# Performance work log

Measured on AMD Instinct MI355X. Metric: run time of the kernel, lower is better.

## Reference

```python
import jax, jax.numpy as jnp
import numpy as np

N_NODES = 50000
N_EDGES = 1600000
IN_FEAT = 48
OUT_FEAT = 48
NUM_RELS = 8


def setup_inputs() -> dict:
    key = jax.random.key(0)
    ks = jax.random.split(key, 9)
    # xavier-ish scale for relu gain
    s1 = float(np.sqrt(2.0) * np.sqrt(6.0 / (IN_FEAT + IN_FEAT)))
    s2 = float(np.sqrt(2.0) * np.sqrt(6.0 / (IN_FEAT + OUT_FEAT)))
    return {
        "inputs": jax.random.normal(ks[0], (N_NODES, IN_FEAT), dtype=jnp.float32),
        "norm": jax.random.uniform(ks[1], (N_EDGES, 1), dtype=jnp.float32),
        "weight1": jax.random.uniform(ks[2], (NUM_RELS, IN_FEAT, IN_FEAT), jnp.float32, -s1, s1),
        "weight2": jax.random.uniform(ks[3], (NUM_RELS, IN_FEAT, OUT_FEAT), jnp.float32, -s2, s2),
        "bias1": jax.random.normal(ks[4], (IN_FEAT,), dtype=jnp.float32) * 0.1,
        "bias2": jax.random.normal(ks[5], (OUT_FEAT,), dtype=jnp.float32) * 0.1,
        "src": jax.random.randint(ks[6], (N_EDGES,), 0, N_NODES, dtype=jnp.int64) if jax.config.jax_enable_x64 else jax.random.randint(ks[6], (N_EDGES,), 0, N_NODES).astype(jnp.int32),
        "dst": jax.random.randint(ks[7], (N_EDGES,), 0, N_NODES).astype(jnp.int32),
        "rel_type": jax.random.randint(ks[8], (N_EDGES,), 0, NUM_RELS).astype(jnp.int32),
    }


def reference(inputs, norm, weight1, weight2, bias1, bias2, src, dst, rel_type):
    # Message depends only on (src node, relation): precompute per (node, rel).
    # Stage 1: h1[n,r,:] = relu(h[n] @ W1[r] + b1)   -> [N, R, in]
    h1 = jax.nn.relu(jnp.einsum('ni,rij->nrj', inputs, weight1) + bias1)
    # Stage 2: h2[n,r,:] = h1[n,r] @ W2[r]           -> [N, R, out]
    h2 = jnp.einsum('nrj,rjo->nro', h1, weight2)
    # Per-edge gather + norm scaling                 -> [E, out]
    msg = h2[src, rel_type] * norm
    # Scatter-sum aggregation to destination nodes   -> [N, out]
    agg = jax.ops.segment_sum(msg, dst, num_segments=inputs.shape[0])
    # apply_func: bias2 + activation
    return jax.nn.relu(agg + bias2)
```

## Files before the change

kernel.cpp:

```cpp
#include <hip/hip_runtime.h>

#define NN 50000
#define EE 1600000
#define FF 48
#define RR 8
#define H2_ROW 64
#define LSTR 72
#define CAP 96

#define XB 3125
#define WB 8
#define ZB 49
#define K1GRID (XB + WB + ZB)

#define H2TILES 391
#define H2BLKS (H2TILES * RR)
#define K2GRID (H2BLKS * 3)

typedef __attribute__((ext_vector_type(8))) short frag8;
typedef __attribute__((ext_vector_type(4))) float frag4f;

__device__ inline unsigned short bf16r(float f) {
    unsigned u = __float_as_uint(f);
    return (unsigned short)((u + 0x7FFFu + ((u >> 16) & 1u)) >> 16);
}
__device__ inline unsigned bf16pack2(float a, float b) {
    return (unsigned)bf16r(a) | ((unsigned)bf16r(b) << 16);
}

__global__ __launch_bounds__(256) void pre_kernel(
    const float* __restrict__ X, const float* __restrict__ W1,
    const float* __restrict__ W2, unsigned short* __restrict__ Xb,
    unsigned short* __restrict__ W1t, unsigned short* __restrict__ W2t,
    int* __restrict__ count)
{
    int b = blockIdx.x;
    if (b < XB) {
        int g = b * 256 + threadIdx.x;
        int seg = g & 15;
        uint2 v = make_uint2(0u, 0u);
        if (seg < 12) {
            float4 x = ((const float4*)X)[(size_t)(g >> 4) * 12 + seg];
            v = make_uint2(bf16pack2(x.x, x.y), bf16pack2(x.z, x.w));
        }
        ((uint2*)Xb)[g] = v;
        return;
    }
    if (b < XB + WB) {
        int r = b - XB;
        const float* w1 = W1 + (size_t)r * FF * FF;
        const float* w2 = W2 + (size_t)r * FF * FF;
        for (int idx = threadIdx.x; idx < 48 * 64; idx += 256) {
            int j = idx >> 6, k = idx & 63;
            W1t[(size_t)r * 48 * 64 + idx] = (k < FF) ? bf16r(w1[k * FF + j]) : (unsigned short)0;
            W2t[(size_t)r * 48 * 64 + idx] = (k < FF) ? bf16r(w2[k * FF + j]) : (unsigned short)0;
        }
        return;
    }
    int z = (b - XB - WB) * 256 + threadIdx.x;
    if (z < 12500) ((int4*)count)[z] = make_int4(0, 0, 0, 0);
}

__global__ __launch_bounds__(256) void h2_place_kernel(
    const unsigned short* __restrict__ Xb, const unsigned short* __restrict__ W1t,
    const unsigned short* __restrict__ W2t, const float* __restrict__ B1,
    const int* __restrict__ srcv, const int* __restrict__ dstv,
    const int* __restrict__ relv, const float* __restrict__ norm,
    int* __restrict__ count, unsigned* __restrict__ payload,
    unsigned short* __restrict__ H2)
{
    __shared__ unsigned short h1s[128 * LSTR];
    int b = blockIdx.x;
    int bmod = b - (b / 3) * 3;
    if (bmod != 0) {
        int p = (b / 3) * 2 + bmod - 1;
        int e = p * 256 + threadIdx.x;
        if (e < EE) {
            int d = dstv[e];
            int pos = atomicAdd(&count[d], 1);
            unsigned qn = (unsigned)(norm[e] * 8192.0f + 0.5f);
            if (qn > 8191u) qn = 8191u;
            unsigned rec = ((unsigned)(srcv[e] * 8 + relv[e]) << 13) | qn;
            if ((unsigned)pos < (unsigned)CAP)
                __builtin_nontemporal_store(rec, &payload[(size_t)d * CAP + pos]);
        }
        return;
    }
    int h    = b / 3;
    int r    = h & 7;
    int tile = h >> 3;
    int tid  = threadIdx.x;
    int w    = tid >> 6, ln = tid & 63, q = ln >> 4, lq = ln & 15;
    int nb   = tile * 128 + w * 32;

    unsigned short* myh1 = &h1s[(w * 32) * LSTR];
    for (int i = ln; i < 32 * 12; i += 64) {
        int rr = i / 12, cs = i - rr * 12;
        *(unsigned*)&myh1[rr * LSTR + 48 + cs * 2] = 0;
    }

    int row0 = nb + lq;      if (row0 >= NN) row0 = NN - 1;
    int row1 = nb + 16 + lq; if (row1 >= NN) row1 = NN - 1;
    const frag8 a00 = *(const frag8*)&Xb[(size_t)row0 * 64 + q * 8];
    const frag8 a01 = *(const frag8*)&Xb[(size_t)row0 * 64 + 32 + q * 8];
    const frag8 a10 = *(const frag8*)&Xb[(size_t)row1 * 64 + q * 8];
    const frag8 a11 = *(const frag8*)&Xb[(size_t)row1 * 64 + 32 + q * 8];

    const unsigned short* w1r = W1t + (size_t)r * 48 * 64;
    const unsigned short* w2r = W2t + (size_t)r * 48 * 64;

    #pragma unroll
    for (int t = 0; t < 3; ++t) {
        int col = t * 16 + lq;
        frag8 b0 = *(const frag8*)&w1r[(col << 6) + q * 8];
        frag8 b1 = *(const frag8*)&w1r[(col << 6) + 32 + q * 8];
        float bc = B1[col];
        frag4f acc0 = {bc, bc, bc, bc};
        frag4f acc1 = {bc, bc, bc, bc};
        acc0 = __builtin_amdgcn_mfma_f32_16x16x32_bf16(a00, b0, acc0, 0, 0, 0);
        acc0 = __builtin_amdgcn_mfma_f32_16x16x32_bf16(a01, b1, acc0, 0, 0, 0);
        acc1 = __builtin_amdgcn_mfma_f32_16x16x32_bf16(a10, b0, acc1, 0, 0, 0);
        acc1 = __builtin_amdgcn_mfma_f32_16x16x32_bf16(a11, b1, acc1, 0, 0, 0);
        #pragma unroll
        for (int g = 0; g < 4; ++g) {
            myh1[(q * 4 + g) * LSTR + col]      = bf16r(fmaxf(acc0[g], 0.0f));
            myh1[(16 + q * 4 + g) * LSTR + col] = bf16r(fmaxf(acc1[g], 0.0f));
        }
    }

    const frag8 c00 = *(const frag8*)&myh1[lq * LSTR + q * 8];
    const frag8 c01 = *(const frag8*)&myh1[lq * LSTR + 32 + q * 8];
    const frag8 c10 = *(const frag8*)&myh1[(16 + lq) * LSTR + q * 8];
    const frag8 c11 = *(const frag8*)&myh1[(16 + lq) * LSTR + 32 + q * 8];

    #pragma unroll
    for (int t = 0; t < 3; ++t) {
        int col = t * 16 + lq;
        frag8 b0 = *(const frag8*)&w2r[(col << 6) + q * 8];
        frag8 b1 = *(const frag8*)&w2r[(col << 6) + 32 + q * 8];
        frag4f acc0 = {0.f, 0.f, 0.f, 0.f};
        frag4f acc1 = {0.f, 0.f, 0.f, 0.f};
        acc0 = __builtin_amdgcn_mfma_f32_16x16x32_bf16(c00, b0, acc0, 0, 0, 0);
        acc0 = __builtin_amdgcn_mfma_f32_16x16x32_bf16(c01, b1, acc0, 0, 0, 0);
        acc1 = __builtin_amdgcn_mfma_f32_16x16x32_bf16(c10, b0, acc1, 0, 0, 0);
        acc1 = __builtin_amdgcn_mfma_f32_16x16x32_bf16(c11, b1, acc1, 0, 0, 0);
        #pragma unroll
        for (int g = 0; g < 4; ++g) {
            int n0 = nb + q * 4 + g;
            int n1 = nb + 16 + q * 4 + g;
            if (n0 < NN) H2[((size_t)n0 * RR + r) * H2_ROW + col] = bf16r(acc0[g]);
            if (n1 < NN) H2[((size_t)n1 * RR + r) * H2_ROW + col] = bf16r(acc1[g]);
        }
    }
}

__global__ __launch_bounds__(256) void gather_kernel(
    const unsigned short* __restrict__ H2, const unsigned* __restrict__ payload,
    const int* __restrict__ count, const float* __restrict__ B2,
    float* __restrict__ out)
{
    unsigned tid = blockIdx.x * 256u + threadIdx.x;
    unsigned n = tid / 12u;
    unsigned c = tid - n * 12u;
    if (n >= NN) return;

    int cnt = count[n];
    if (cnt > CAP) cnt = CAP;
    if (cnt < 0) cnt = 0;
    const unsigned* pl = payload + (size_t)n * CAP;
    float a0 = 0.f, a1 = 0.f, a2 = 0.f, a3 = 0.f;
    for (int e = 0; e < cnt; ++e) {
        unsigned p = pl[e];
        float nm = (float)(p & 8191u) * (1.0f / 8192.0f);
        const uint2* row = (const uint2*)(H2 + (size_t)(p >> 13) * H2_ROW);
        uint2 v = row[c];
        a0 = fmaf(__uint_as_float(v.x << 16),         nm, a0);
        a1 = fmaf(__uint_as_float(v.x & 0xFFFF0000u), nm, a1);
        a2 = fmaf(__uint_as_float(v.y << 16),         nm, a2);
        a3 = fmaf(__uint_as_float(v.y & 0xFFFF0000u), nm, a3);
    }
    float4 b = ((const float4*)B2)[c];
    ((float4*)out)[(size_t)n * 12u + c] = make_float4(
        fmaxf(a0 + b.x, 0.f), fmaxf(a1 + b.y, 0.f),
        fmaxf(a2 + b.z, 0.f), fmaxf(a3 + b.w, 0.f));
}

extern "C" void kernel_launch(void* const* d_in, const int* in_sizes, int n_in,
                              void* d_out, int out_size, void* d_ws, size_t ws_size,
                              hipStream_t stream) {
    const float* X   = (const float*)d_in[0];
    const float* nrm = (const float*)d_in[1];
    const float* W1  = (const float*)d_in[2];
    const float* W2  = (const float*)d_in[3];
    const float* B1  = (const float*)d_in[4];
    const float* B2  = (const float*)d_in[5];
    const int*   src = (const int*)d_in[6];
    const int*   dst = (const int*)d_in[7];
    const int*   rel = (const int*)d_in[8];
    float* out = (float*)d_out;

    unsigned short* H2      = (unsigned short*)d_ws;
    unsigned*       payload = (unsigned*)(H2 + (size_t)NN * RR * H2_ROW);
    unsigned short* Xb      = (unsigned short*)(payload + (size_t)NN * CAP);
    unsigned short* W1t     = Xb + (size_t)NN * 64;
    unsigned short* W2t     = W1t + RR * 48 * 64;
    int*            count   = (int*)(W2t + RR * 48 * 64);

    pre_kernel<<<K1GRID, 256, 0, stream>>>(X, W1, W2, Xb, W1t, W2t, count);

    h2_place_kernel<<<K2GRID, 256, 0, stream>>>(
        Xb, W1t, W2t, B1, src, dst, rel, nrm, count, payload, H2);

    unsigned total = (unsigned)NN * 12u;
    gather_kernel<<<(total + 255) / 256, 256, 0, stream>>>(
        H2, payload, count, B2, out);
}
```

Baseline: 253.9 us.

## Bucket edges by 64-node destination tile and accumulate in shared memory

Replaces the per-destination-node CSR-like payload, which uses one global atomic per node, with per-tile, per-segment buckets holding a local node index, a src*8+rel index and the full fp32 norm. The gather kernel now processes one 64-node tile per block and accumulates messages into shared memory with LDS float atomics. The intent is to spread global atomic contention over 8 segment cursors per tile and get better coalescing and parallelism in the gather. The cost is LDS atomic contention, 8-byte records instead of 4, and a hard per-segment cap of 448 edges, beyond which edges are silently dropped.

```diff
diff --git a/kernel.cpp b/kernel.cpp
--- a/kernel.cpp
+++ b/kernel.cpp
@@ -6,11 +6,15 @@
 #define RR 8
 #define H2_ROW 64
 #define LSTR 72
-#define CAP 96
+
+#define NT 782
+#define SEG 8
+#define SCAP 448
+#define CURS 16
 
 #define XB 3125
 #define WB 8
-#define ZB 49
+#define ZB 13
 #define K1GRID (XB + WB + ZB)
 
 #define H2TILES 391
@@ -32,7 +36,7 @@
     const float* __restrict__ X, const float* __restrict__ W1,
     const float* __restrict__ W2, unsigned short* __restrict__ Xb,
     unsigned short* __restrict__ W1t, unsigned short* __restrict__ W2t,
-    int* __restrict__ count)
+    int* __restrict__ cursor)
 {
     int b = blockIdx.x;
     if (b < XB) {
@@ -58,7 +62,7 @@
         return;
     }
     int z = (b - XB - WB) * 256 + threadIdx.x;
-    if (z < 12500) ((int4*)count)[z] = make_int4(0, 0, 0, 0);
+    if (z < 3128) ((int4*)cursor)[z] = make_int4(0, 0, 0, 0);
 }
 
 __global__ __launch_bounds__(256) void h2_place_kernel(
@@ -66,7 +70,7 @@
     const unsigned short* __restrict__ W2t, const float* __restrict__ B1,
     const int* __restrict__ srcv, const int* __restrict__ dstv,
     const int* __restrict__ relv, const float* __restrict__ norm,
-    int* __restrict__ count, unsigned* __restrict__ payload,
+    int* __restrict__ cursor, uint2* __restrict__ bucket,
     unsigned short* __restrict__ H2)
 {
     __shared__ unsigned short h1s[128 * LSTR];
@@ -77,12 +81,15 @@
         int e = p * 256 + threadIdx.x;
         if (e < EE) {
             int d = dstv[e];
-            int pos = atomicAdd(&count[d], 1);
-            unsigned qn = (unsigned)(norm[e] * 8192.0f + 0.5f);
-            if (qn > 8191u) qn = 8191u;
-            unsigned rec = ((unsigned)(srcv[e] * 8 + relv[e]) << 13) | qn;
-            if ((unsigned)pos < (unsigned)CAP)
-                __builtin_nontemporal_store(rec, &payload[(size_t)d * CAP + pos]);
+            int tile = d >> 6;
+            int seg = b & 7;
+            int pos = atomicAdd(&cursor[tile * CURS + seg], 1);
+            if (pos < SCAP) {
+                unsigned meta = ((unsigned)(d & 63) << 19) |
+                                (unsigned)(srcv[e] * 8 + relv[e]);
+                bucket[((size_t)(tile * SEG + seg)) * SCAP + pos] =
+                    make_uint2(meta, __float_as_uint(norm[e]));
+            }
         }
         return;
     }
@@ -155,34 +162,59 @@
 }
 
 __global__ __launch_bounds__(256) void gather_kernel(
-    const unsigned short* __restrict__ H2, const unsigned* __restrict__ payload,
-    const int* __restrict__ count, const float* __restrict__ B2,
+    const unsigned short* __restrict__ H2, const uint2* __restrict__ bucket,
+    const int* __restrict__ cursor, const float* __restrict__ B2,
     float* __restrict__ out)
 {
-    unsigned tid = blockIdx.x * 256u + threadIdx.x;
-    unsigned n = tid / 12u;
-    unsigned c = tid - n * 12u;
-    if (n >= NN) return;
-
-    int cnt = count[n];
-    if (cnt > CAP) cnt = CAP;
-    if (cnt < 0) cnt = 0;
-    const unsigned* pl = payload + (size_t)n * CAP;
-    float a0 = 0.f, a1 = 0.f, a2 = 0.f, a3 = 0.f;
-    for (int e = 0; e < cnt; ++e) {
-        unsigned p = pl[e];
-        float nm = (float)(p & 8191u) * (1.0f / 8192.0f);
-        const uint2* row = (const uint2*)(H2 + (size_t)(p >> 13) * H2_ROW);
-        uint2 v = row[c];
-        a0 = fmaf(__uint_as_float(v.x << 16),         nm, a0);
-        a1 = fmaf(__uint_as_float(v.x & 0xFFFF0000u), nm, a1);
-        a2 = fmaf(__uint_as_float(v.y << 16),         nm, a2);
-        a3 = fmaf(__uint_as_float(v.y & 0xFFFF0000u), nm, a3);
-    }
-    float4 b = ((const float4*)B2)[c];
-    ((float4*)out)[(size_t)n * 12u + c] = make_float4(
-        fmaxf(a0 + b.x, 0.f), fmaxf(a1 + b.y, 0.f),
-        fmaxf(a2 + b.z, 0.f), fmaxf(a3 + b.w, 0.f));
+    __shared__ float acc[64 * 49];
+    int tile = blockIdx.x;
+    int tid = threadIdx.x;
+    for (int i = tid; i < 64 * 49; i += 256) acc[i] = 0.0f;
+    __syncthreads();
+
+    int team = tid / 12;
+    int c = tid - team * 12;
+    if (team < 21) {
+        for (int seg = 0; seg < SEG; ++seg) {
+            int cnt = cursor[tile * CURS + seg];
+            if (cnt > SCAP) cnt = SCAP;
+            const uint2* bk = bucket + ((size_t)(tile * SEG + seg)) * SCAP;
+            int e = team;
+            for (; e + 63 < cnt; e += 84) {
+                uint2 r0 = bk[e], r1 = bk[e + 21], r2 = bk[e + 42], r3 = bk[e + 63];
+                uint2 v0 = ((const uint2*)(H2 + (size_t)(r0.x & 0x7FFFFu) * H2_ROW))[c];
+                uint2 v1 = ((const uint2*)(H2 + (size_t)(r1.x & 0x7FFFFu) * H2_ROW))[c];
+                uint2 v2 = ((const uint2*)(H2 + (size_t)(r2.x & 0x7FFFFu) * H2_ROW))[c];
+                uint2 v3 = ((const uint2*)(H2 + (size_t)(r3.x & 0x7FFFFu) * H2_ROW))[c];
+                #define ACCUM(rr, vv) {                                          \
+                    float nm = __uint_as_float(rr.y);                            \
+                    float* a = &acc[(rr.x >> 19) * 49 + c * 4];                  \
+                    atomicAdd(a + 0, __uint_as_float(vv.x << 16) * nm);          \
+                    atomicAdd(a + 1, __uint_as_float(vv.x & 0xFFFF0000u) * nm);  \
+                    atomicAdd(a + 2, __uint_as_float(vv.y << 16) * nm);          \
+                    atomicAdd(a + 3, __uint_as_float(vv.y & 0xFFFF0000u) * nm); }
+                ACCUM(r0, v0) ACCUM(r1, v1) ACCUM(r2, v2) ACCUM(r3, v3)
+            }
+            for (; e < cnt; e += 21) {
+                uint2 r0 = bk[e];
+                uint2 v0 = ((const uint2*)(H2 + (size_t)(r0.x & 0x7FFFFu) * H2_ROW))[c];
+                ACCUM(r0, v0)
+            }
+        }
+    }
+    __syncthreads();
+
+    for (int i = tid; i < 768; i += 256) {
+        int local = i / 12, cc = i - local * 12;
+        int n = tile * 64 + local;
+        if (n < NN) {
+            float4 bb = ((const float4*)B2)[cc];
+            float* a = &acc[local * 49 + cc * 4];
+            ((float4*)out)[(size_t)n * 12 + cc] = make_float4(
+                fmaxf(a[0] + bb.x, 0.f), fmaxf(a[1] + bb.y, 0.f),
+                fmaxf(a[2] + bb.z, 0.f), fmaxf(a[3] + bb.w, 0.f));
+        }
+    }
 }
 
 extern "C" void kernel_launch(void* const* d_in, const int* in_sizes, int n_in,
@@ -199,19 +231,17 @@
     const int*   rel = (const int*)d_in[8];
     float* out = (float*)d_out;
 
-    unsigned short* H2      = (unsigned short*)d_ws;
-    unsigned*       payload = (unsigned*)(H2 + (size_t)NN * RR * H2_ROW);
-    unsigned short* Xb      = (unsigned short*)(payload + (size_t)NN * CAP);
-    unsigned short* W1t     = Xb + (size_t)NN * 64;
-    unsigned short* W2t     = W1t + RR * 48 * 64;
-    int*            count   = (int*)(W2t + RR * 48 * 64);
-
-    pre_kernel<<<K1GRID, 256, 0, stream>>>(X, W1, W2, Xb, W1t, W2t, count);
+    unsigned short* H2     = (unsigned short*)d_ws;
+    uint2*          bucket = (uint2*)(H2 + (size_t)NN * RR * H2_ROW);
+    unsigned short* Xb     = (unsigned short*)(bucket + (size_t)NT * SEG * SCAP);
+    unsigned short* W1t    = Xb + (size_t)NN * 64;
+    unsigned short* W2t    = W1t + RR * 48 * 64;
+    int*            cursor = (int*)(W2t + RR * 48 * 64);
+
+    pre_kernel<<<K1GRID, 256, 0, stream>>>(X, W1, W2, Xb, W1t, W2t, cursor);
 
     h2_place_kernel<<<K2GRID, 256, 0, stream>>>(
-        Xb, W1t, W2t, B1, src, dst, rel, nrm, count, payload, H2);
-
-    unsigned total = (unsigned)NN * 12u;
-    gather_kernel<<<(total + 255) / 256, 256, 0, stream>>>(
-        H2, payload, count, B2, out);
-}
+        Xb, W1t, W2t, B1, src, dst, rel, nrm, cursor, bucket, H2);
+
+    gather_kernel<<<NT, 256, 0, stream>>>(H2, bucket, cursor, B2, out);
+}
```

After: 682.1 us. 2.69x slower.
